# Kernel tuning notes

Hardware: AMD Instinct MI355X
Metric: run time of the kernel (lower is better)

Reference implementation:

```python
import jax, jax.numpy as jnp
import numpy as np


def setup_inputs() -> dict:
    key = jax.random.key(0)
    x = jax.random.normal(key, (2, 2048, 512), dtype=jnp.float32)
    return {"x": x, "num_heads": 8, "kernel_size": 63}


def reference(x, num_heads, kernel_size):
    # NATTEN na1d with dilation=1: each query attends to a kernel_size window
    # centered at its position; near the sequence edges the window is shifted
    # (clamped) to stay fully inside [0, L), so every query sees exactly K keys.
    B, L, D = x.shape
    H = num_heads
    hd = D // H
    K = kernel_size
    scale = float(hd) ** -0.5

    qkv = x.reshape(B, L, H, hd)  # q == k == v == reshaped x

    # window start per query position, clamped so the window fits in bounds
    start = jnp.clip(jnp.arange(L) - K // 2, 0, L - K)          # (L,)
    idx = start[:, None] + jnp.arange(K)                         # (L, K)

    kv = qkv[:, idx]                                             # (B, L, K, H, hd)
    scores = jnp.einsum("blhd,blkhd->bhlk", qkv, kv) * scale     # (B, H, L, K)
    attn = jax.nn.softmax(scores, axis=-1)
    out = jnp.einsum("bhlk,blkhd->blhd", attn, kv)               # (B, L, H, hd)
    return out.reshape(B, L, D)
```

## Files before the change

kernel.cpp:

```cpp
#include <hip/hip_runtime.h>

#define B_ 2
#define L_ 2048
#define H_ 8
#define HD 64
#define K_ 63
#define TQ 64
#define NT (L_ / TQ)
#define ROWS 128
#define EXPC 0.1803368801111204f

typedef __attribute__((ext_vector_type(8))) short bf16x8;
typedef __attribute__((ext_vector_type(4))) float f32x4;

__device__ inline unsigned cvt_pk_bf16(float lo, float hi) {
    unsigned r;
    asm("v_cvt_pk_bf16_f32 %0, %1, %2" : "=v"(r) : "v"(lo), "v"(hi));
    return r;
}

__global__ __launch_bounds__(256, 2) void natten1d_mfma(
    const float* __restrict__ x, float* __restrict__ out)
{
    __shared__ unsigned short kv_sh [ROWS * 64];
    __shared__ unsigned short kvT_sh[64 * ROWS];
    __shared__ unsigned short pt_sh [4 * 16 * 128];

    const int bid = blockIdx.x;
    const int wid = (bid & 7) * (B_ * H_ * NT / 8) + (bid >> 3);
    const int bh  = wid / NT;
    const int t   = wid % NT;
    const int b   = bh / H_;
    const int h   = bh % H_;
    const int l0  = t * TQ;
    const int key_base = min(max(l0 - K_ / 2, 0), L_ - K_);
    const int qoff     = l0 - key_base;

    const int tid = threadIdx.x;
    const int c   = tid & 7;
    const int rw  = tid >> 3;

    const float4* xb = (const float4*)x + (size_t)b * (L_ * H_ * HD / 4) + h * (HD / 4);
    float4 la[4], lb[4];
    #pragma unroll
    for (int rr = 0; rr < 4; ++rr) {
        const int g = key_base + rw * 4 + rr;
        const bool ok = (g < L_);
        const size_t ro = (size_t)g * (H_ * HD / 4);
        la[rr] = ok ? xb[ro + c]     : make_float4(0.f, 0.f, 0.f, 0.f);
        lb[rr] = ok ? xb[ro + c + 8] : make_float4(0.f, 0.f, 0.f, 0.f);
    }

    #pragma unroll
    for (int rr = 0; rr < 4; ++rr) {
        const int r = rw * 4 + rr;
        uint2 w;
        w.x = cvt_pk_bf16(la[rr].x, la[rr].y);
        w.y = cvt_pk_bf16(la[rr].z, la[rr].w);
        *(uint2*)&kv_sh[r * 64 + (((c >> 1) ^ (r & 7)) << 3) + (c & 1) * 4] = w;
    }
    {
        const int key = rw * 4;
        const float* f0 = (const float*)&la[0];
        const float* f1 = (const float*)&la[1];
        const float* f2 = (const float*)&la[2];
        const float* f3 = (const float*)&la[3];
        #pragma unroll
        for (int e = 0; e < 4; ++e) {
            const int d = c * 4 + e;
            uint2 w;
            w.x = cvt_pk_bf16(f0[e], f1[e]);
            w.y = cvt_pk_bf16(f2[e], f3[e]);
            *(uint2*)&kvT_sh[d * 128 + (((key >> 3) ^ (d & 15)) << 3) + (key & 7)] = w;
        }
    }
    __syncthreads();

    const int wave = tid >> 6;
    const int lane = tid & 63;
    const int lq = lane & 15;
    const int lg = lane >> 4;

    const int q0    = wave * 16;
    const int soff0 = min(max(l0 + q0 - K_ / 2, 0), L_ - K_) - key_base;
    const int wb    = min(soff0 & ~15, ROWS - 96);
    const int qrow  = qoff + q0 + lq;
    const int soffq = min(max(l0 + q0 + lq - K_ / 2, 0), L_ - K_) - key_base;
    const int cbase = wb + lg * 4 - soffq;

    f32x4 acc[6];
    #pragma unroll
    for (int nb = 0; nb < 6; ++nb) acc[nb] = (f32x4){0.f, 0.f, 0.f, 0.f};
    {
        const bf16x8 bq0 = *(const bf16x8*)&kv_sh[qrow * 64 + ((lg ^ (qrow & 7)) << 3)];
        #pragma unroll
        for (int nb = 0; nb < 6; ++nb) {
            const int krow = wb + nb * 16 + lq;
            const bf16x8 a0 = *(const bf16x8*)&kv_sh[krow * 64 + ((lg ^ (krow & 7)) << 3)];
            acc[nb] = __builtin_amdgcn_mfma_f32_16x16x32_bf16(a0, bq0, acc[nb], 0, 0, 0);
        }
    }

    #pragma unroll
    for (int rr = 0; rr < 4; ++rr) {
        const int r = rw * 4 + rr;
        uint2 w;
        w.x = cvt_pk_bf16(lb[rr].x, lb[rr].y);
        w.y = cvt_pk_bf16(lb[rr].z, lb[rr].w);
        *(uint2*)&kv_sh[r * 64 + ((((c >> 1) + 4) ^ (r & 7)) << 3) + (c & 1) * 4] = w;
    }
    {
        const int key = rw * 4;
        const float* f0 = (const float*)&lb[0];
        const float* f1 = (const float*)&lb[1];
        const float* f2 = (const float*)&lb[2];
        const float* f3 = (const float*)&lb[3];
        #pragma unroll
        for (int e = 0; e < 4; ++e) {
            const int d = 32 + c * 4 + e;
            uint2 w;
            w.x = cvt_pk_bf16(f0[e], f1[e]);
            w.y = cvt_pk_bf16(f2[e], f3[e]);
            *(uint2*)&kvT_sh[d * 128 + (((key >> 3) ^ (d & 15)) << 3) + (key & 7)] = w;
        }
    }
    __syncthreads();

    {
        const bf16x8 bq1 = *(const bf16x8*)&kv_sh[qrow * 64 + (((4 + lg) ^ (qrow & 7)) << 3)];
        #pragma unroll
        for (int nb = 0; nb < 6; ++nb) {
            const int krow = wb + nb * 16 + lq;
            const bf16x8 a1 = *(const bf16x8*)&kv_sh[krow * 64 + (((4 + lg) ^ (krow & 7)) << 3)];
            acc[nb] = __builtin_amdgcn_mfma_f32_16x16x32_bf16(a1, bq1, acc[nb], 0, 0, 0);
        }
    }

    float mx = -1e30f;
    #pragma unroll
    for (int nb = 0; nb < 6; ++nb) {
        #pragma unroll
        for (int r = 0; r < 4; ++r) {
            const bool valid = (unsigned)(cbase + nb * 16 + r) < (unsigned)K_;
            const float s = valid ? acc[nb][r] : -1e30f;
            acc[nb][r] = s;
            mx = fmaxf(mx, s);
        }
    }
    mx = fmaxf(mx, __shfl_xor(mx, 16));
    mx = fmaxf(mx, __shfl_xor(mx, 32));
    float z = 0.f;
    #pragma unroll
    for (int nb = 0; nb < 6; ++nb) {
        #pragma unroll
        for (int r = 0; r < 4; ++r) {
            const float e = exp2f((acc[nb][r] - mx) * EXPC);
            acc[nb][r] = e;
            z += e;
        }
    }
    z += __shfl_xor(z, 16);
    z += __shfl_xor(z, 32);
    const float rz = 1.0f / z;

    unsigned short* ptw = &pt_sh[wave * 16 * 128];
    #pragma unroll
    for (int nb = 0; nb < 6; ++nb) {
        uint2 w;
        w.x = cvt_pk_bf16(acc[nb][0] * rz, acc[nb][1] * rz);
        w.y = cvt_pk_bf16(acc[nb][2] * rz, acc[nb][3] * rz);
        const int g = nb * 2 + (lg >> 1);
        *(uint2*)&ptw[lq * 128 + ((g ^ lq) << 3) + ((lg & 1) << 2)] = w;
    }

    bf16x8 ap[3];
    #pragma unroll
    for (int kc = 0; kc < 3; ++kc)
        ap[kc] = *(const bf16x8*)&ptw[lq * 128 + (((kc * 4 + lg) ^ lq) << 3)];
    f32x4 o4[4];
    #pragma unroll
    for (int nb = 0; nb < 4; ++nb) o4[nb] = (f32x4){0.f, 0.f, 0.f, 0.f};
    const int kg0 = wb >> 3;
    #pragma unroll
    for (int nb = 0; nb < 4; ++nb) {
        const int d = nb * 16 + lq;
        #pragma unroll
        for (int kc = 0; kc < 3; ++kc) {
            const bf16x8 bv =
                *(const bf16x8*)&kvT_sh[d * 128 + (((kg0 + kc * 4 + lg) ^ (d & 15)) << 3)];
            o4[nb] = __builtin_amdgcn_mfma_f32_16x16x32_bf16(ap[kc], bv, o4[nb], 0, 0, 0);
        }
    }

    #pragma unroll
    for (int nb = 0; nb < 4; ++nb) {
        const int d = nb * 16 + lq;
        #pragma unroll
        for (int r = 0; r < 4; ++r) {
            const int q = q0 + lg * 4 + r;
            out[((size_t)(b * L_ + l0 + q) * H_ + h) * HD + d] = o4[nb][r];
        }
    }
}

extern "C" void kernel_launch(void* const* d_in, const int* in_sizes, int n_in,
                              void* d_out, int out_size, void* d_ws, size_t ws_size,
                              hipStream_t stream)
{
    const float* x = (const float*)d_in[0];
    float* out = (float*)d_out;
    natten1d_mfma<<<dim3(B_ * H_ * NT), dim3(256), 0, stream>>>(x, out);
}
```

Baseline: 10.65 us.

## Split key window across two wave halves with flash-style softmax merge

Doubles the block to 512 threads. Each query group's 96-key window is split between two waves, 64 keys and 32 keys, and each computes a partial softmax and a partial PV product. The second half writes its partial output as bf16 into shared memory along with per-row max and sum. The first half then rescales and combines the two partials before writing the output. The intent is more waves per block for better latency hiding and shorter per-wave chains, at the cost of an extra barrier, uneven work between the halves, and bf16 rounding of the partial output.

Result: slower. 11.57 us (+8.7%).

```diff
diff --git a/kernel.cpp b/kernel.cpp
--- a/kernel.cpp
+++ b/kernel.cpp
@@ -18,13 +18,23 @@
     asm("v_cvt_pk_bf16_f32 %0, %1, %2" : "=v"(r) : "v"(lo), "v"(hi));
     return r;
 }
-
-__global__ __launch_bounds__(256, 2) void natten1d_mfma(
+__device__ inline unsigned short f2bf(float f) {
+    unsigned u = __float_as_uint(f);
+    unsigned r = ((u >> 16) & 1u) + 0x7FFFu;
+    return (unsigned short)((u + r) >> 16);
+}
+__device__ inline float bf2f(unsigned short s) {
+    return __uint_as_float(((unsigned)s) << 16);
+}
+
+__global__ __launch_bounds__(512, 4) void natten1d_mfma(
     const float* __restrict__ x, float* __restrict__ out)
 {
     __shared__ unsigned short kv_sh [ROWS * 64];
     __shared__ unsigned short kvT_sh[64 * ROWS];
-    __shared__ unsigned short pt_sh [4 * 16 * 128];
+    __shared__ unsigned short pt_sh [8 * 16 * 64];
+    __shared__ float2 mz0_sh[4][16];
+    __shared__ float2 mz1_sh[4][16];
 
     const int bid = blockIdx.x;
     const int wid = (bid & 7) * (B_ * H_ * NT / 8) + (bid >> 3);
@@ -41,10 +51,10 @@
     const int rw  = tid >> 3;
 
     const float4* xb = (const float4*)x + (size_t)b * (L_ * H_ * HD / 4) + h * (HD / 4);
-    float4 la[4], lb[4];
-    #pragma unroll
-    for (int rr = 0; rr < 4; ++rr) {
-        const int g = key_base + rw * 4 + rr;
+    float4 la[2], lb[2];
+    #pragma unroll
+    for (int rr = 0; rr < 2; ++rr) {
+        const int g = key_base + rw * 2 + rr;
         const bool ok = (g < L_);
         const size_t ro = (size_t)g * (H_ * HD / 4);
         la[rr] = ok ? xb[ro + c]     : make_float4(0.f, 0.f, 0.f, 0.f);
@@ -52,96 +62,109 @@
     }
 
     #pragma unroll
-    for (int rr = 0; rr < 4; ++rr) {
-        const int r = rw * 4 + rr;
+    for (int rr = 0; rr < 2; ++rr) {
+        const int r = rw * 2 + rr;
         uint2 w;
         w.x = cvt_pk_bf16(la[rr].x, la[rr].y);
         w.y = cvt_pk_bf16(la[rr].z, la[rr].w);
         *(uint2*)&kv_sh[r * 64 + (((c >> 1) ^ (r & 7)) << 3) + (c & 1) * 4] = w;
     }
     {
-        const int key = rw * 4;
         const float* f0 = (const float*)&la[0];
         const float* f1 = (const float*)&la[1];
-        const float* f2 = (const float*)&la[2];
-        const float* f3 = (const float*)&la[3];
         #pragma unroll
         for (int e = 0; e < 4; ++e) {
             const int d = c * 4 + e;
-            uint2 w;
-            w.x = cvt_pk_bf16(f0[e], f1[e]);
-            w.y = cvt_pk_bf16(f2[e], f3[e]);
-            *(uint2*)&kvT_sh[d * 128 + (((key >> 3) ^ (d & 15)) << 3) + (key & 7)] = w;
+            *(unsigned*)&kvT_sh[d * 128 + (((rw >> 2) ^ (d & 15)) << 3) + ((rw & 3) << 1)]
+                = cvt_pk_bf16(f0[e], f1[e]);
         }
     }
     __syncthreads();
 
     const int wave = tid >> 6;
+    const int qg   = wave & 3;
+    const int half = wave >> 2;
     const int lane = tid & 63;
     const int lq = lane & 15;
     const int lg = lane >> 4;
 
-    const int q0    = wave * 16;
+    const int q0    = qg * 16;
     const int soff0 = min(max(l0 + q0 - K_ / 2, 0), L_ - K_) - key_base;
     const int wb    = min(soff0 & ~15, ROWS - 96);
     const int qrow  = qoff + q0 + lq;
     const int soffq = min(max(l0 + q0 + lq - K_ / 2, 0), L_ - K_) - key_base;
     const int cbase = wb + lg * 4 - soffq;
 
-    f32x4 acc[6];
-    #pragma unroll
-    for (int nb = 0; nb < 6; ++nb) acc[nb] = (f32x4){0.f, 0.f, 0.f, 0.f};
+    f32x4 acc[4];
+    #pragma unroll
+    for (int nb = 0; nb < 4; ++nb) acc[nb] = (f32x4){0.f, 0.f, 0.f, 0.f};
     {
         const bf16x8 bq0 = *(const bf16x8*)&kv_sh[qrow * 64 + ((lg ^ (qrow & 7)) << 3)];
-        #pragma unroll
-        for (int nb = 0; nb < 6; ++nb) {
-            const int krow = wb + nb * 16 + lq;
-            const bf16x8 a0 = *(const bf16x8*)&kv_sh[krow * 64 + ((lg ^ (krow & 7)) << 3)];
-            acc[nb] = __builtin_amdgcn_mfma_f32_16x16x32_bf16(a0, bq0, acc[nb], 0, 0, 0);
-        }
-    }
-
-    #pragma unroll
-    for (int rr = 0; rr < 4; ++rr) {
-        const int r = rw * 4 + rr;
+        if (half == 0) {
+            #pragma unroll
+            for (int nb = 0; nb < 4; ++nb) {
+                const int krow = wb + nb * 16 + lq;
+                const bf16x8 a0 = *(const bf16x8*)&kv_sh[krow * 64 + ((lg ^ (krow & 7)) << 3)];
+                acc[nb] = __builtin_amdgcn_mfma_f32_16x16x32_bf16(a0, bq0, acc[nb], 0, 0, 0);
+            }
+        } else {
+            #pragma unroll
+            for (int nb = 0; nb < 2; ++nb) {
+                const int krow = wb + (4 + nb) * 16 + lq;
+                const bf16x8 a0 = *(const bf16x8*)&kv_sh[krow * 64 + ((lg ^ (krow & 7)) << 3)];
+                acc[nb] = __builtin_amdgcn_mfma_f32_16x16x32_bf16(a0, bq0, acc[nb], 0, 0, 0);
+            }
+        }
+    }
+
+    #pragma unroll
+    for (int rr = 0; rr < 2; ++rr) {
+        const int r = rw * 2 + rr;
         uint2 w;
         w.x = cvt_pk_bf16(lb[rr].x, lb[rr].y);
         w.y = cvt_pk_bf16(lb[rr].z, lb[rr].w);
         *(uint2*)&kv_sh[r * 64 + ((((c >> 1) + 4) ^ (r & 7)) << 3) + (c & 1) * 4] = w;
     }
     {
-        const int key = rw * 4;
         const float* f0 = (const float*)&lb[0];
         const float* f1 = (const float*)&lb[1];
-        const float* f2 = (const float*)&lb[2];
-        const float* f3 = (const float*)&lb[3];
         #pragma unroll
         for (int e = 0; e < 4; ++e) {
             const int d = 32 + c * 4 + e;
-            uint2 w;
-            w.x = cvt_pk_bf16(f0[e], f1[e]);
-            w.y = cvt_pk_bf16(f2[e], f3[e]);
-            *(uint2*)&kvT_sh[d * 128 + (((key >> 3) ^ (d & 15)) << 3) + (key & 7)] = w;
+            *(unsigned*)&kvT_sh[d * 128 + (((rw >> 2) ^ (d & 15)) << 3) + ((rw & 3) << 1)]
+                = cvt_pk_bf16(f0[e], f1[e]);
         }
     }
     __syncthreads();
 
     {
         const bf16x8 bq1 = *(const bf16x8*)&kv_sh[qrow * 64 + (((4 + lg) ^ (qrow & 7)) << 3)];
-        #pragma unroll
-        for (int nb = 0; nb < 6; ++nb) {
-            const int krow = wb + nb * 16 + lq;
-            const bf16x8 a1 = *(const bf16x8*)&kv_sh[krow * 64 + (((4 + lg) ^ (krow & 7)) << 3)];
-            acc[nb] = __builtin_amdgcn_mfma_f32_16x16x32_bf16(a1, bq1, acc[nb], 0, 0, 0);
-        }
-    }
-
+        if (half == 0) {
+            #pragma unroll
+            for (int nb = 0; nb < 4; ++nb) {
+                const int krow = wb + nb * 16 + lq;
+                const bf16x8 a1 = *(const bf16x8*)&kv_sh[krow * 64 + (((4 + lg) ^ (krow & 7)) << 3)];
+                acc[nb] = __builtin_amdgcn_mfma_f32_16x16x32_bf16(a1, bq1, acc[nb], 0, 0, 0);
+            }
+        } else {
+            #pragma unroll
+            for (int nb = 0; nb < 2; ++nb) {
+                const int krow = wb + (4 + nb) * 16 + lq;
+                const bf16x8 a1 = *(const bf16x8*)&kv_sh[krow * 64 + (((4 + lg) ^ (krow & 7)) << 3)];
+                acc[nb] = __builtin_amdgcn_mfma_f32_16x16x32_bf16(a1, bq1, acc[nb], 0, 0, 0);
+            }
+        }
+    }
+
+    const int NBH = (half == 0) ? 4 : 2;
     float mx = -1e30f;
     #pragma unroll
-    for (int nb = 0; nb < 6; ++nb) {
+    for (int nb = 0; nb < 4; ++nb) {
+        if (nb >= NBH) break;
+        const int nbg = half * 4 + nb;
         #pragma unroll
         for (int r = 0; r < 4; ++r) {
-            const bool valid = (unsigned)(cbase + nb * 16 + r) < (unsigned)K_;
+            const bool valid = (unsigned)(cbase + nbg * 16 + r) < (unsigned)K_;
             const float s = valid ? acc[nb][r] : -1e30f;
             acc[nb][r] = s;
             mx = fmaxf(mx, s);
@@ -151,7 +174,8 @@
     mx = fmaxf(mx, __shfl_xor(mx, 32));
     float z = 0.f;
     #pragma unroll
-    for (int nb = 0; nb < 6; ++nb) {
+    for (int nb = 0; nb < 4; ++nb) {
+        if (nb >= NBH) break;
         #pragma unroll
         for (int r = 0; r < 4; ++r) {
             const float e = exp2f((acc[nb][r] - mx) * EXPC);
@@ -161,44 +185,86 @@
     }
     z += __shfl_xor(z, 16);
     z += __shfl_xor(z, 32);
-    const float rz = 1.0f / z;
-
-    unsigned short* ptw = &pt_sh[wave * 16 * 128];
-    #pragma unroll
-    for (int nb = 0; nb < 6; ++nb) {
+
+    if (lg == 0) {
+        if (half == 0) mz0_sh[qg][lq] = make_float2(mx, z);
+        else           mz1_sh[qg][lq] = make_float2(mx, z);
+    }
+
+    unsigned short* ptw = &pt_sh[wave * 16 * 64];
+    #pragma unroll
+    for (int nb = 0; nb < 4; ++nb) {
+        if (nb >= NBH) break;
         uint2 w;
-        w.x = cvt_pk_bf16(acc[nb][0] * rz, acc[nb][1] * rz);
-        w.y = cvt_pk_bf16(acc[nb][2] * rz, acc[nb][3] * rz);
+        w.x = cvt_pk_bf16(acc[nb][0], acc[nb][1]);
+        w.y = cvt_pk_bf16(acc[nb][2], acc[nb][3]);
         const int g = nb * 2 + (lg >> 1);
-        *(uint2*)&ptw[lq * 128 + ((g ^ lq) << 3) + ((lg & 1) << 2)] = w;
-    }
-
-    bf16x8 ap[3];
-    #pragma unroll
-    for (int kc = 0; kc < 3; ++kc)
-        ap[kc] = *(const bf16x8*)&ptw[lq * 128 + (((kc * 4 + lg) ^ lq) << 3)];
+        *(uint2*)&ptw[lq * 64 + ((g ^ (lq & 7)) << 3) + ((lg & 1) << 2)] = w;
+    }
+
     f32x4 o4[4];
     #pragma unroll
-    for (int nb = 0; nb < 4; ++nb) o4[nb] = (f32x4){0.f, 0.f, 0.f, 0.f};
-    const int kg0 = wb >> 3;
-    #pragma unroll
-    for (int nb = 0; nb < 4; ++nb) {
-        const int d = nb * 16 + lq;
-        #pragma unroll
-        for (int kc = 0; kc < 3; ++kc) {
-            const bf16x8 bv =
-                *(const bf16x8*)&kvT_sh[d * 128 + (((kg0 + kc * 4 + lg) ^ (d & 15)) << 3)];
-            o4[nb] = __builtin_amdgcn_mfma_f32_16x16x32_bf16(ap[kc], bv, o4[nb], 0, 0, 0);
-        }
-    }
-
-    #pragma unroll
-    for (int nb = 0; nb < 4; ++nb) {
-        const int d = nb * 16 + lq;
+    for (int nb2 = 0; nb2 < 4; ++nb2) o4[nb2] = (f32x4){0.f, 0.f, 0.f, 0.f};
+    if (half == 0) {
+        bf16x8 ap0 = *(const bf16x8*)&ptw[lq * 64 + (((0 * 4 + lg) ^ (lq & 7)) << 3)];
+        bf16x8 ap1 = *(const bf16x8*)&ptw[lq * 64 + (((1 * 4 + lg) ^ (lq & 7)) << 3)];
+        #pragma unroll
+        for (int nb2 = 0; nb2 < 4; ++nb2) {
+            const int d = nb2 * 16 + lq;
+            const int g0 = ((wb >> 3) + lg)     ^ (d & 15);
+            const int g1 = ((wb >> 3) + 4 + lg) ^ (d & 15);
+            const bf16x8 bv0 = *(const bf16x8*)&kvT_sh[d * 128 + (g0 << 3)];
+            const bf16x8 bv1 = *(const bf16x8*)&kvT_sh[d * 128 + (g1 << 3)];
+            o4[nb2] = __builtin_amdgcn_mfma_f32_16x16x32_bf16(ap0, bv0, o4[nb2], 0, 0, 0);
+            o4[nb2] = __builtin_amdgcn_mfma_f32_16x16x32_bf16(ap1, bv1, o4[nb2], 0, 0, 0);
+        }
+    } else {
+        bf16x8 ap0 = *(const bf16x8*)&ptw[lq * 64 + ((lg ^ (lq & 7)) << 3)];
+        #pragma unroll
+        for (int nb2 = 0; nb2 < 4; ++nb2) {
+            const int d = nb2 * 16 + lq;
+            const int g0 = ((wb >> 3) + 8 + lg) ^ (d & 15);
+            const bf16x8 bv0 = *(const bf16x8*)&kvT_sh[d * 128 + (g0 << 3)];
+            o4[nb2] = __builtin_amdgcn_mfma_f32_16x16x32_bf16(ap0, bv0, o4[nb2], 0, 0, 0);
+        }
+        unsigned short* ofw = ptw;
+        #pragma unroll
+        for (int nb2 = 0; nb2 < 4; ++nb2) {
+            const int d = nb2 * 16 + lq;
+            #pragma unroll
+            for (int r = 0; r < 4; ++r) {
+                const int q = lg * 4 + r;
+                ofw[q * 64 + (d ^ (lg << 3))] = f2bf(o4[nb2][r]);
+            }
+        }
+    }
+    __syncthreads();
+
+    if (half == 0) {
+        const unsigned short* ofr = &pt_sh[(4 + qg) * 16 * 64];
+        float c0[4], c1[4];
         #pragma unroll
         for (int r = 0; r < 4; ++r) {
-            const int q = q0 + lg * 4 + r;
-            out[((size_t)(b * L_ + l0 + q) * H_ + h) * HD + d] = o4[nb][r];
+            const int q = lg * 4 + r;
+            const float2 a  = mz0_sh[qg][q];
+            const float2 bz = mz1_sh[qg][q];
+            const float m  = fmaxf(a.x, bz.x);
+            const float e0 = exp2f((a.x - m) * EXPC);
+            const float e1 = exp2f((bz.x - m) * EXPC);
+            const float rz = 1.0f / (e0 * a.y + e1 * bz.y);
+            c0[r] = e0 * rz;
+            c1[r] = e1 * rz;
+        }
+        #pragma unroll
+        for (int nb2 = 0; nb2 < 4; ++nb2) {
+            const int d = nb2 * 16 + lq;
+            #pragma unroll
+            for (int r = 0; r < 4; ++r) {
+                const int q = lg * 4 + r;
+                const float o1 = bf2f(ofr[q * 64 + (d ^ (lg << 3))]);
+                out[((size_t)(b * L_ + l0 + q0 + q) * H_ + h) * HD + d]
+                    = c0[r] * o4[nb2][r] + c1[r] * o1;
+            }
         }
     }
 }
@@ -209,5 +275,5 @@
 {
     const float* x = (const float*)d_in[0];
     float* out = (float*)d_out;
-    natten1d_mfma<<<dim3(B_ * H_ * NT), dim3(256), 0, stream>>>(x, out);
-}
+    natten1d_mfma<<<dim3(B_ * H_ * NT), dim3(512), 0, stream>>>(x, out);
+}
```
